# Kernel optimization log

Hardware: AMD Instinct MI355X
Metric: run time of the kernel (lower is better)

The kernel has to match this reference:

```python
import jax, jax.numpy as jnp
import numpy as np

B, TE, TD, D, U = 8, 256, 256, 256, 256


def setup_inputs() -> dict:
    key = jax.random.key(0)
    k1, k2, k3, k4, k5 = jax.random.split(key, 5)
    glorot = lambda k, shape: jax.random.uniform(
        k, shape, jnp.float32,
        -np.sqrt(6.0 / (shape[0] + shape[1])), np.sqrt(6.0 / (shape[0] + shape[1])))
    return {
        "en_seq": jax.random.normal(k1, (B, TE, D), jnp.float32),
        "de_seq": jax.random.normal(k2, (B, TD, D), jnp.float32),
        "w_en": glorot(k3, (D, U)),
        "w_de": glorot(k4, (D, U)),
        "nu": glorot(k5, (U, 1)),
    }


def reference(en_seq, de_seq, w_en, w_de, nu):
    # Additive co-attention scores.
    ae = jnp.einsum('bte,eu->btu', en_seq, w_en)          # (B, Te, U)
    ad = jnp.einsum('bsd,du->bsu', de_seq, w_de)          # (B, Td, U)
    # co_m[b, td, te, u] = ae[b, te, u] + ad[b, td, u]  (matches K.repeat / repeat_elements layout)
    co = jnp.tanh(ad[:, :, None, :] + ae[:, None, :, :])  # (B, Td, Te, U)
    mu = jnp.einsum('bstu,ul->bst', co, nu)               # (B, Td, Te)
    alphas = jax.nn.softmax(mu, axis=-1)                  # softmax over en time
    max_mu = jnp.max(mu, axis=-1)                         # (B, Td)
    max_alphas = jax.nn.softmax(max_mu, axis=-1)          # softmax over de time
    h_hat = jnp.sum(de_seq * max_alphas[..., None], axis=1)  # (B, Dd)
    sum_en = jnp.einsum('bst,bte->bse', alphas, en_seq)      # (B, Td, De)
    output = jnp.concatenate(
        [de_seq, sum_en, de_seq * sum_en, de_seq * h_hat[:, None, :]], axis=-1)
    return output  # (B, Td, 4*D)
```

## Files before the change

kernel.cpp:

```cpp
#include <hip/hip_runtime.h>

#define B_   8
#define TE_  256
#define TD_  256
#define D_   256
#define U_   256

#define EET_OFF   0
#define ED_OFF    524288
#define MAXMU_OFF 1048576

__device__ __forceinline__ float fexp2(float x) {
#if __has_builtin(__builtin_amdgcn_exp2f)
  return __builtin_amdgcn_exp2f(x);
#else
  return exp2f(x);
#endif
}
__device__ __forceinline__ float frcp(float x) {
#if __has_builtin(__builtin_amdgcn_rcpf)
  return __builtin_amdgcn_rcpf(x);
#else
  return 1.0f / x;
#endif
}

#define LOG2E_F 1.4426950408889634f
#define TWO_LOG2E_F 2.8853900817779268f

__global__ __launch_bounds__(512) void coatt_k1_proj(
    const float* __restrict__ en, const float* __restrict__ de,
    const float* __restrict__ w_en, const float* __restrict__ w_de,
    float* __restrict__ eet, float* __restrict__ edp) {
  const int which = blockIdx.z;
  const float* __restrict__ A = which ? de : en;
  const float* __restrict__ W = which ? w_de : w_en;
  const int rowBase = blockIdx.y * 64;
  const int colBase = blockIdx.x * 32;
  __shared__ float Bs[256][32];
  const int tid = threadIdx.x;
  const int tx = tid & 15, ty = tid >> 4;

  {
    const int r = tid >> 1, h = (tid & 1) * 16;
#pragma unroll
    for (int j = 0; j < 4; ++j)
      *(float4*)&Bs[r][h + j * 4] =
          *(const float4*)&W[(size_t)r * U_ + colBase + h + j * 4];
  }
  __syncthreads();

  float acc[2][2] = {};
#pragma unroll 4
  for (int k4 = 0; k4 < 64; ++k4) {
    float a0[4], a1[4];
    *(float4*)a0 = *(const float4*)&A[(size_t)(rowBase + ty * 2 + 0) * D_ + k4 * 4];
    *(float4*)a1 = *(const float4*)&A[(size_t)(rowBase + ty * 2 + 1) * D_ + k4 * 4];
#pragma unroll
    for (int kk = 0; kk < 4; ++kk) {
      float b[2];
      *(float2*)b = *(const float2*)&Bs[k4 * 4 + kk][tx * 2];
      acc[0][0] = fmaf(a0[kk], b[0], acc[0][0]);
      acc[0][1] = fmaf(a0[kk], b[1], acc[0][1]);
      acc[1][0] = fmaf(a1[kk], b[0], acc[1][0]);
      acc[1][1] = fmaf(a1[kk], b[1], acc[1][1]);
    }
  }

  if (which) {
#pragma unroll
    for (int i = 0; i < 2; ++i) {
      float2 o;
      o.x = fexp2(acc[i][0] * TWO_LOG2E_F);
      o.y = fexp2(acc[i][1] * TWO_LOG2E_F);
      *(float2*)&edp[(size_t)(rowBase + ty * 2 + i) * U_ + colBase + tx * 2] = o;
    }
  } else {
    __syncthreads();
    float* Cs = &Bs[0][0];
#pragma unroll
    for (int i = 0; i < 2; ++i)
#pragma unroll
      for (int j = 0; j < 2; ++j)
        Cs[(tx * 2 + j) * 69 + ty * 2 + i] = fexp2(acc[i][j] * TWO_LOG2E_F);
    __syncthreads();
    const int b = rowBase >> 8, t0 = rowBase & 255;
    const int u4Base = colBase >> 2;
    const int u4l = tid >> 6, tl = tid & 63;
    float4 v;
    v.x = Cs[(u4l * 4 + 0) * 69 + tl];
    v.y = Cs[(u4l * 4 + 1) * 69 + tl];
    v.z = Cs[(u4l * 4 + 2) * 69 + tl];
    v.w = Cs[(u4l * 4 + 3) * 69 + tl];
    *(float4*)&eet[(size_t)((b * 64 + u4Base + u4l) * 256 + t0 + tl) * 4] = v;
  }
}

__global__ __launch_bounds__(512) void coatt_k24(
    const float* __restrict__ en, const float* __restrict__ de,
    const float* __restrict__ nu, const float* __restrict__ eet,
    const float* __restrict__ edp, float* __restrict__ maxmu,
    float* __restrict__ out) {
  const int id = blockIdx.x;
  const int b = id & 7;
  const int sBase = (id >> 3) * 4;
  const int tid = threadIdx.x;
  const int t = tid & 255;
  const int half = tid >> 8;
  const int w = tid >> 6, lane = tid & 63;

  __shared__ float als[4][256];
  __shared__ float tp[2][4][256];
  __shared__ float part[2][8];

  const int edBase =
      __builtin_amdgcn_readfirstlane((b * TD_ + sBase + half * 2) * U_);
  const float* __restrict__ Ed0 = edp + edBase;
  const float* __restrict__ Ed1 = Ed0 + U_;
  const float* __restrict__ Ee_b = eet + (size_t)b * (U_ * TE_) + t * 4;

  float accA0 = 0.f, accB0 = 0.f, accA1 = 0.f, accB1 = 0.f;
#pragma unroll 4
  for (int u4 = 0; u4 < 64; ++u4) {
    const float4 ee4 = *(const float4*)&Ee_b[u4 * 1024];
    const float4 nv = *(const float4*)&nu[u4 * 4];
    const float4 d0 = *(const float4*)&Ed0[u4 * 4];
    const float4 d1 = *(const float4*)&Ed1[u4 * 4];
    const float* eep = (const float*)&ee4;
    const float* nvp = (const float*)&nv;
    const float* p0 = (const float*)&d0;
    const float* p1 = (const float*)&d1;
#pragma unroll
    for (int j = 0; j < 4; ++j) {
      const float r0 = frcp(fmaf(p0[j], eep[j], 1.0f));
      const float r1 = frcp(fmaf(p1[j], eep[j], 1.0f));
      if (j & 1) {
        accB0 = fmaf(nvp[j], r0, accB0);
        accB1 = fmaf(nvp[j], r1, accB1);
      } else {
        accA0 = fmaf(nvp[j], r0, accA0);
        accA1 = fmaf(nvp[j], r1, accA1);
      }
    }
  }
  float v0 = -2.f * (accA0 + accB0);
  float v1 = -2.f * (accA1 + accB1);

  float m0 = v0, m1 = v1;
#pragma unroll
  for (int off = 32; off > 0; off >>= 1) {
    m0 = fmaxf(m0, __shfl_xor(m0, off));
    m1 = fmaxf(m1, __shfl_xor(m1, off));
  }
  if (lane == 0) { part[0][w] = m0; part[1][w] = m1; }
  __syncthreads();
  const int wb = half * 4;
  m0 = fmaxf(fmaxf(part[0][wb], part[0][wb + 1]),
             fmaxf(part[0][wb + 2], part[0][wb + 3]));
  m1 = fmaxf(fmaxf(part[1][wb], part[1][wb + 1]),
             fmaxf(part[1][wb + 2], part[1][wb + 3]));
  __syncthreads();
  const float e0 = fexp2((v0 - m0) * LOG2E_F);
  const float e1 = fexp2((v1 - m1) * LOG2E_F);
  float sm0 = e0, sm1 = e1;
#pragma unroll
  for (int off = 32; off > 0; off >>= 1) {
    sm0 += __shfl_xor(sm0, off);
    sm1 += __shfl_xor(sm1, off);
  }
  if (lane == 0) { part[0][w] = sm0; part[1][w] = sm1; }
  __syncthreads();
  const float tot0 = (part[0][wb] + part[0][wb + 1]) +
                     (part[0][wb + 2] + part[0][wb + 3]);
  const float tot1 = (part[1][wb] + part[1][wb + 1]) +
                     (part[1][wb + 2] + part[1][wb + 3]);
  const int s0 = half * 2;
  als[s0][t] = e0 * frcp(tot0);
  als[s0 + 1][t] = e1 * frcp(tot1);
  if (t == 0) {
    maxmu[b * TD_ + sBase + s0] = m0;
    maxmu[b * TD_ + sBase + s0 + 1] = m1;
  }
  __syncthreads();

  const int d = t;
  const int tBeg = half * 128;
  const float* __restrict__ en_b = en + (size_t)b * TE_ * D_ + d;
  float sa0 = 0.f, sa1 = 0.f, sa2 = 0.f, sa3 = 0.f;
#pragma unroll 4
  for (int t4 = 0; t4 < 32; ++t4) {
    const int tt = tBeg + t4 * 4;
    const float4 a0 = *(const float4*)&als[0][tt];
    const float4 a1 = *(const float4*)&als[1][tt];
    const float4 a2 = *(const float4*)&als[2][tt];
    const float4 a3 = *(const float4*)&als[3][tt];
    float env[4];
#pragma unroll
    for (int j = 0; j < 4; ++j) env[j] = en_b[(size_t)(tt + j) * D_];
    const float* q0 = (const float*)&a0;
    const float* q1 = (const float*)&a1;
    const float* q2 = (const float*)&a2;
    const float* q3 = (const float*)&a3;
#pragma unroll
    for (int j = 0; j < 4; ++j) {
      sa0 = fmaf(q0[j], env[j], sa0);
      sa1 = fmaf(q1[j], env[j], sa1);
      sa2 = fmaf(q2[j], env[j], sa2);
      sa3 = fmaf(q3[j], env[j], sa3);
    }
  }
  tp[half][0][d] = sa0;
  tp[half][1][d] = sa1;
  tp[half][2][d] = sa2;
  tp[half][3][d] = sa3;
  __syncthreads();
#pragma unroll
  for (int k = 0; k < 2; ++k) {
    const int sl = s0 + k;
    const float se = tp[0][sl][d] + tp[1][sl][d];
    const int s = sBase + sl;
    const float dd = de[(size_t)(b * TD_ + s) * D_ + d];
    float* o = out + (size_t)(b * TD_ + s) * (4 * D_);
    o[d] = dd;
    o[D_ + d] = se;
    o[2 * D_ + d] = dd * se;
  }
}

__global__ __launch_bounds__(256) void coatt_k3_hhat(
    const float* __restrict__ de, const float* __restrict__ maxmu,
    float* __restrict__ out) {
  const int b = blockIdx.y;
  const int dBase = blockIdx.x * 32;
  const int tid = threadIdx.x;
  const int w = tid >> 6, lane = tid & 63;
  __shared__ float red[8];
  __shared__ float malpha[256];
  __shared__ float acc_red[256];
  __shared__ float hh_s[32];
  const float vv = maxmu[b * TD_ + tid];
  float m = vv;
#pragma unroll
  for (int off = 32; off > 0; off >>= 1) m = fmaxf(m, __shfl_xor(m, off));
  if (lane == 0) red[w] = m;
  __syncthreads();
  m = fmaxf(fmaxf(red[0], red[1]), fmaxf(red[2], red[3]));
  const float e = fexp2((vv - m) * LOG2E_F);
  float sm = e;
#pragma unroll
  for (int off = 32; off > 0; off >>= 1) sm += __shfl_xor(sm, off);
  if (lane == 0) red[4 + w] = sm;
  __syncthreads();
  sm = (red[4] + red[5]) + (red[6] + red[7]);
  malpha[tid] = e * frcp(sm);
  __syncthreads();
  const int dl = tid & 31, sg = tid >> 5;
  float acc = 0.f;
  for (int s = sg * 32; s < sg * 32 + 32; ++s)
    acc = fmaf(de[(size_t)(b * TD_ + s) * D_ + dBase + dl], malpha[s], acc);
  acc_red[tid] = acc;
  __syncthreads();
  if (tid < 32) {
    float tsum = acc_red[tid];
#pragma unroll
    for (int g = 1; g < 8; ++g) tsum += acc_red[g * 32 + tid];
    hh_s[tid] = tsum;
  }
  __syncthreads();
  const float hh = hh_s[dl];
#pragma unroll 4
  for (int s = sg; s < TD_; s += 8) {
    const float dd = de[(size_t)(b * TD_ + s) * D_ + dBase + dl];
    out[(size_t)(b * TD_ + s) * (4 * D_) + 3 * D_ + dBase + dl] = dd * hh;
  }
}

extern "C" void kernel_launch(void* const* d_in, const int* in_sizes, int n_in,
                              void* d_out, int out_size, void* d_ws, size_t ws_size,
                              hipStream_t stream) {
  (void)in_sizes; (void)n_in; (void)out_size; (void)ws_size;
  const float* en   = (const float*)d_in[0];
  const float* de   = (const float*)d_in[1];
  const float* w_en = (const float*)d_in[2];
  const float* w_de = (const float*)d_in[3];
  const float* nu   = (const float*)d_in[4];
  float* out = (float*)d_out;
  float* ws  = (float*)d_ws;

  coatt_k1_proj<<<dim3(8, 32, 2), 512, 0, stream>>>(
      en, de, w_en, w_de, ws + EET_OFF, ws + ED_OFF);
  coatt_k24<<<dim3(512), 512, 0, stream>>>(
      en, de, nu, ws + EET_OFF, ws + ED_OFF, ws + MAXMU_OFF, out);
  coatt_k3_hhat<<<dim3(8, 8), 256, 0, stream>>>(de, ws + MAXMU_OFF, out);
}
```

Measured before the change: 113.7 us.

## Fuse h_hat kernel into attention kernel via last-block atomic counter

Removes the separate h_hat kernel launch. Each attention block now bumps a per-batch atomic counter, and the last block to finish for a batch computes the softmax over max_mu, h_hat, and the fourth output slice. The counters are zeroed in the projection kernel. This saves one launch and its dependency gap, but the whole per-batch tail is serialized onto a single 512-thread block per batch, which reads all of de twice.

```diff
diff --git a/kernel.cpp b/kernel.cpp
--- a/kernel.cpp
+++ b/kernel.cpp
@@ -9,6 +9,7 @@
 #define EET_OFF   0
 #define ED_OFF    524288
 #define MAXMU_OFF 1048576
+#define CNT_OFF   1050624
 
 __device__ __forceinline__ float fexp2(float x) {
 #if __has_builtin(__builtin_amdgcn_exp2f)
@@ -31,7 +32,7 @@
 __global__ __launch_bounds__(512) void coatt_k1_proj(
     const float* __restrict__ en, const float* __restrict__ de,
     const float* __restrict__ w_en, const float* __restrict__ w_de,
-    float* __restrict__ eet, float* __restrict__ edp) {
+    float* __restrict__ eet, float* __restrict__ edp, int* __restrict__ cnt) {
   const int which = blockIdx.z;
   const float* __restrict__ A = which ? de : en;
   const float* __restrict__ W = which ? w_de : w_en;
@@ -40,6 +41,9 @@
   __shared__ float Bs[256][32];
   const int tid = threadIdx.x;
   const int tx = tid & 15, ty = tid >> 4;
+
+  if (which == 0 && blockIdx.x == 0 && blockIdx.y == 0 && tid < 8)
+    cnt[tid] = 0;
 
   {
     const int r = tid >> 1, h = (tid & 1) * 16;
@@ -100,7 +104,7 @@
     const float* __restrict__ en, const float* __restrict__ de,
     const float* __restrict__ nu, const float* __restrict__ eet,
     const float* __restrict__ edp, float* __restrict__ maxmu,
-    float* __restrict__ out) {
+    int* __restrict__ cnt, float* __restrict__ out) {
   const int id = blockIdx.x;
   const int b = id & 7;
   const int sBase = (id >> 3) * 4;
@@ -112,6 +116,7 @@
   __shared__ float als[4][256];
   __shared__ float tp[2][4][256];
   __shared__ float part[2][8];
+  __shared__ int lastFlag;
 
   const int edBase =
       __builtin_amdgcn_readfirstlane((b * TD_ + sBase + half * 2) * U_);
@@ -225,53 +230,48 @@
     o[D_ + d] = se;
     o[2 * D_ + d] = dd * se;
   }
-}
-
-__global__ __launch_bounds__(256) void coatt_k3_hhat(
-    const float* __restrict__ de, const float* __restrict__ maxmu,
-    float* __restrict__ out) {
-  const int b = blockIdx.y;
-  const int dBase = blockIdx.x * 32;
-  const int tid = threadIdx.x;
-  const int w = tid >> 6, lane = tid & 63;
-  __shared__ float red[8];
-  __shared__ float malpha[256];
-  __shared__ float acc_red[256];
-  __shared__ float hh_s[32];
-  const float vv = maxmu[b * TD_ + tid];
-  float m = vv;
-#pragma unroll
-  for (int off = 32; off > 0; off >>= 1) m = fmaxf(m, __shfl_xor(m, off));
-  if (lane == 0) red[w] = m;
-  __syncthreads();
-  m = fmaxf(fmaxf(red[0], red[1]), fmaxf(red[2], red[3]));
-  const float e = fexp2((vv - m) * LOG2E_F);
-  float sm = e;
-#pragma unroll
-  for (int off = 32; off > 0; off >>= 1) sm += __shfl_xor(sm, off);
-  if (lane == 0) red[4 + w] = sm;
-  __syncthreads();
-  sm = (red[4] + red[5]) + (red[6] + red[7]);
-  malpha[tid] = e * frcp(sm);
-  __syncthreads();
-  const int dl = tid & 31, sg = tid >> 5;
-  float acc = 0.f;
-  for (int s = sg * 32; s < sg * 32 + 32; ++s)
-    acc = fmaf(de[(size_t)(b * TD_ + s) * D_ + dBase + dl], malpha[s], acc);
-  acc_red[tid] = acc;
-  __syncthreads();
-  if (tid < 32) {
-    float tsum = acc_red[tid];
-#pragma unroll
-    for (int g = 1; g < 8; ++g) tsum += acc_red[g * 32 + tid];
-    hh_s[tid] = tsum;
-  }
-  __syncthreads();
-  const float hh = hh_s[dl];
-#pragma unroll 4
-  for (int s = sg; s < TD_; s += 8) {
-    const float dd = de[(size_t)(b * TD_ + s) * D_ + dBase + dl];
-    out[(size_t)(b * TD_ + s) * (4 * D_) + 3 * D_ + dBase + dl] = dd * hh;
+
+  if (tid == 0) {
+    __threadfence();
+    const int old = __hip_atomic_fetch_add(&cnt[b], 1, __ATOMIC_ACQ_REL,
+                                           __HIP_MEMORY_SCOPE_AGENT);
+    lastFlag = (old == 63);
+  }
+  __syncthreads();
+  if (lastFlag) {
+    __threadfence();
+    float* ma = als[0];
+    const float vv = maxmu[b * TD_ + t];
+    float m2 = vv;
+#pragma unroll
+    for (int off = 32; off > 0; off >>= 1) m2 = fmaxf(m2, __shfl_xor(m2, off));
+    if (lane == 0) part[0][w] = m2;
+    __syncthreads();
+    m2 = fmaxf(fmaxf(fmaxf(part[0][0], part[0][1]), fmaxf(part[0][2], part[0][3])),
+               fmaxf(fmaxf(part[0][4], part[0][5]), fmaxf(part[0][6], part[0][7])));
+    const float e2 = fexp2((vv - m2) * LOG2E_F);
+    float sm2 = e2;
+#pragma unroll
+    for (int off = 32; off > 0; off >>= 1) sm2 += __shfl_xor(sm2, off);
+    if (lane == 0) part[1][w] = sm2;
+    __syncthreads();
+    const float tot2 = 0.5f * (((part[1][0] + part[1][1]) + (part[1][2] + part[1][3])) +
+                               ((part[1][4] + part[1][5]) + (part[1][6] + part[1][7])));
+    ma[t] = e2 * frcp(tot2);
+    __syncthreads();
+    const float* __restrict__ de_b = de + (size_t)b * TD_ * D_ + t;
+    float acc = 0.f;
+#pragma unroll 4
+    for (int s = half * 128; s < half * 128 + 128; ++s)
+      acc = fmaf(de_b[(size_t)s * D_], ma[s], acc);
+    tp[half][0][t] = acc;
+    __syncthreads();
+    const float hh = tp[0][0][t] + tp[1][0][t];
+#pragma unroll 4
+    for (int s = half * 128; s < half * 128 + 128; ++s) {
+      const float dd = de_b[(size_t)s * D_];
+      out[(size_t)(b * TD_ + s) * (4 * D_) + 3 * D_ + t] = dd * hh;
+    }
   }
 }
 
@@ -286,10 +286,10 @@
   const float* nu   = (const float*)d_in[4];
   float* out = (float*)d_out;
   float* ws  = (float*)d_ws;
+  int* cnt = (int*)(ws + CNT_OFF);
 
   coatt_k1_proj<<<dim3(8, 32, 2), 512, 0, stream>>>(
-      en, de, w_en, w_de, ws + EET_OFF, ws + ED_OFF);
+      en, de, w_en, w_de, ws + EET_OFF, ws + ED_OFF, cnt);
   coatt_k24<<<dim3(512), 512, 0, stream>>>(
-      en, de, nu, ws + EET_OFF, ws + ED_OFF, ws + MAXMU_OFF, out);
-  coatt_k3_hhat<<<dim3(8, 8), 256, 0, stream>>>(de, ws + MAXMU_OFF, out);
-}
+      en, de, nu, ws + EET_OFF, ws + ED_OFF, ws + MAXMU_OFF, cnt, out);
+}
```

Result: slower. 145.1 us (+27.7%).
